# Kernel tuning notes

Hardware: AMD Instinct MI355X
Metric: run time of the kernel (lower is better)

## Reference

```python
import jax, jax.numpy as jnp
import numpy as np
import math

HIDDEN = 1024
HEADS = 16
HEAD_DIM = HIDDEN // HEADS


def setup_inputs() -> dict:
    key = jax.random.key(0)
    k1, k2, k3, k4, k5 = jax.random.split(key, 5)
    B, S = 2, 2048
    scale = 1.0 / math.sqrt(HIDDEN)
    return {
        "batch_hidden": jax.random.normal(k1, (B, S, HIDDEN), dtype=jnp.float32),
        # nn.Linear weights are [out, in]; y = x @ W.T
        "Wq": jax.random.uniform(k2, (HIDDEN, HIDDEN), jnp.float32, -scale, scale),
        "Wk": jax.random.uniform(k3, (HIDDEN, HIDDEN), jnp.float32, -scale, scale),
        "Wg": jax.random.uniform(k4, (HIDDEN, HIDDEN), jnp.float32, -scale, scale),
        "bg": jax.random.uniform(k5, (HIDDEN,), jnp.float32, -scale, scale),
    }


def _split_heads(x):
    # [B,S,H] -> [B,heads,S,head_dim]
    B, S, _ = x.shape
    return x.reshape(B, S, HEADS, HEAD_DIM).transpose(0, 2, 1, 3)


def reference(batch_hidden, Wq, Wk, Wg, bg):
    # NOTE: faithful to source — value uses the KEY projection weights.
    q = batch_hidden @ Wq.T
    k = batch_hidden @ Wk.T
    v = batch_hidden @ Wk.T
    gate = jax.nn.sigmoid(batch_hidden @ Wg.T + bg)  # [B,S,H]

    q = _split_heads(q)  # [B,h,S,d]
    k = _split_heads(k)
    v = _split_heads(v)

    # source: scores = K @ Q^T (softmax over query positions)
    scores = jnp.einsum("bhkd,bhqd->bhkq", k, q) / math.sqrt(HEAD_DIM)
    attn = jax.nn.softmax(scores, axis=-1)  # [B,h,S,S]

    ctx = jnp.einsum("bhkq,bhqd->bhkd", attn, v)  # [B,h,S,d]
    ctx = ctx.transpose(0, 2, 1, 3).reshape(batch_hidden.shape)  # [B,S,H]

    out = gate * ctx
    return out, attn
```

## Files before the change

kernel.cpp:

```cpp
#include <hip/hip_runtime.h>
#include <hip/hip_bf16.h>

#define HID 1024
#define NHEADS 16
#define HDIM 64
#define SEQ 2048
#define NTOK 4096

typedef __attribute__((ext_vector_type(8))) short short8;
typedef __attribute__((ext_vector_type(4))) float f32x4;
typedef unsigned short ush;

__device__ __forceinline__ ush f2bf(float f) {
    unsigned int u = __float_as_uint(f);
    u = (u + 0x7fffu + ((u >> 16) & 1u)) >> 16;
    return (ush)u;
}
__device__ __forceinline__ void async_copy16(const void* g, void* l) {
    __builtin_amdgcn_global_load_lds(
        (const __attribute__((address_space(1))) void*)g,
        (__attribute__((address_space(3))) void*)l, 16, 0, 0);
}
#define SBAR()  __builtin_amdgcn_s_barrier()
#define SCHED() __builtin_amdgcn_sched_barrier(0)

__global__ __launch_bounds__(256) void cvt_kernel(
    const float* __restrict__ X, const float* __restrict__ Wq,
    const float* __restrict__ Wk, const float* __restrict__ Wg,
    ush* __restrict__ Xbf, ush* __restrict__ Wbf)
{
    long i = (long)blockIdx.x * 256 + threadIdx.x;
    const float* src; ush* dst; long j;
    if (i < 524288)      { src = X;  dst = Xbf;           j = i; }
    else if (i < 655360) { src = Wq; dst = Wbf;           j = i - 524288; }
    else if (i < 786432) { src = Wk; dst = Wbf + 1048576; j = i - 655360; }
    else                 { src = Wg; dst = Wbf + 2097152; j = i - 786432; }
    float4 a = *reinterpret_cast<const float4*>(src + j * 8);
    float4 b = *reinterpret_cast<const float4*>(src + j * 8 + 4);
    short8 o;
    o[0] = (short)f2bf(a.x); o[1] = (short)f2bf(a.y);
    o[2] = (short)f2bf(a.z); o[3] = (short)f2bf(a.w);
    o[4] = (short)f2bf(b.x); o[5] = (short)f2bf(b.y);
    o[6] = (short)f2bf(b.z); o[7] = (short)f2bf(b.w);
    *reinterpret_cast<short8*>(dst + j * 8) = o;
}

__global__ __launch_bounds__(256, 3) void proj_kernel(
    const ush* __restrict__ Xbf, const ush* __restrict__ Wbf,
    const float* __restrict__ bgp,
    ush* __restrict__ Qbf, ush* __restrict__ Kbf,
    ush* __restrict__ VtG,
    float* __restrict__ gate)
{
    __shared__ __align__(16) ush As[128 * 64];
    __shared__ __align__(16) ush Bs[128 * 64];

    const int lin = blockIdx.y * 24 + blockIdx.x;
    const int swz = (lin & 7) * 96 + (lin >> 3);
    const int n0 = (swz % 24) * 128;
    const int m0 = (swz / 24) * 128;
    const int tid = threadIdx.x, lane = tid & 63, wv = tid >> 6;
    const int wm = wv >> 1, wn = wv & 1;
    const int l16 = lane & 15, lq = lane >> 4;
    const int lrow = lane >> 3, lc = lane & 7;
    const int scU = lc ^ lrow;
    const int u0 = lq ^ (l16 & 7);

    f32x4 acc[4][4];
    #pragma unroll
    for (int i = 0; i < 4; i++)
        #pragma unroll
        for (int j = 0; j < 4; j++)
            #pragma unroll
            for (int r = 0; r < 4; r++) acc[i][j][r] = 0.0f;

    const ush* gA = Xbf + (long)m0 * HID;
    const ush* gB = Wbf + (long)n0 * HID;

    for (int k0 = 0; k0 < HID; k0 += 64) {
        #pragma unroll
        for (int c = 0; c < 4; ++c) {
            int chunk = wv * 4 + c;
            int row = chunk * 8 + lrow;
            async_copy16(gA + (long)row * HID + k0 + scU * 8, &As[chunk * 512]);
            async_copy16(gB + (long)row * HID + k0 + scU * 8, &Bs[chunk * 512]);
        }
        asm volatile("s_waitcnt vmcnt(0)" ::: "memory");
        SCHED();
        SBAR(); SCHED();
        #pragma unroll
        for (int ks = 0; ks < 2; ++ks) {
            const int uo = (ks ? (u0 ^ 4) : u0) * 8;
            short8 a[4], b[4];
            #pragma unroll
            for (int mf = 0; mf < 4; mf++)
                a[mf] = *reinterpret_cast<const short8*>(&As[(wm * 64 + mf * 16 + l16) * 64 + uo]);
            #pragma unroll
            for (int nf = 0; nf < 4; nf++)
                b[nf] = *reinterpret_cast<const short8*>(&Bs[(wn * 64 + nf * 16 + l16) * 64 + uo]);
            #pragma unroll
            for (int mf = 0; mf < 4; mf++)
                #pragma unroll
                for (int nf = 0; nf < 4; nf++)
                    acc[mf][nf] = __builtin_amdgcn_mfma_f32_16x16x32_bf16(a[mf], b[nf], acc[mf][nf], 0, 0, 0);
        }
        SBAR(); SCHED();
    }

    const int z = n0 >> 10;
    #pragma unroll
    for (int mf = 0; mf < 4; mf++)
        #pragma unroll
        for (int nf = 0; nf < 4; nf++) {
            int row = m0 + wm * 64 + mf * 16 + lq * 4;
            int gcol = n0 + wn * 64 + nf * 16 + l16;
            int col = gcol & 1023;
            #pragma unroll
            for (int r = 0; r < 4; r++) {
                float v = acc[mf][nf][r];
                long idx = (long)(row + r) * HID + col;
                if (z == 0)      Qbf[idx] = f2bf(v * 0.18033688011112042f);
                else if (z == 1) Kbf[idx] = f2bf(v);
                else {
                    float gv = 1.0f / (1.0f + __expf(-(v + bgp[col])));
                    __builtin_nontemporal_store(gv, &gate[idx]);
                }
            }
            if (z == 1) {
                int bb = row >> 11, s = row & 2047;
                int bh = bb * NHEADS + (col >> 6);
                int d  = col & 63;
                unsigned int w0, w1;
                asm volatile("v_cvt_pk_bf16_f32 %0, %1, %2" : "=v"(w0)
                             : "v"(acc[mf][nf][0]), "v"(acc[mf][nf][1]));
                asm volatile("v_cvt_pk_bf16_f32 %0, %1, %2" : "=v"(w1)
                             : "v"(acc[mf][nf][2]), "v"(acc[mf][nf][3]));
                *reinterpret_cast<uint2*>(&VtG[((long)bh * HDIM + d) * SEQ + s]) =
                    make_uint2(w0, w1);
            }
        }
}

__global__ __launch_bounds__(256, 3) void attn_kernel(
    const ush* __restrict__ Qbf,
    const ush* __restrict__ Kbf,
    const ush* __restrict__ VtG,
    float* __restrict__ outp,
    float* __restrict__ attnp)
{
    __shared__ __align__(16) ush QsA[3 * 4096];
    __shared__ __align__(16) ush AtA[128 * 72];
    __shared__ __align__(16) ush VtA[64 * 64];

    ush (*At)[72] = reinterpret_cast<ush(*)[72]>(&AtA[0]);

    const int lin = (blockIdx.z * 16 + blockIdx.y) * 16 + blockIdx.x;
    const int swzb = (lin & 7) * 64 + (lin >> 3);
    const int kblk = swzb & 15;
    const int h    = (swzb >> 4) & 15;
    const int b    = swzb >> 8;
    const int bh   = b * NHEADS + h;
    const int tb   = b * SEQ;
    const int colbase = h * HDIM;
    const int tid  = threadIdx.x;
    const int lane = tid & 63;
    const int wv   = tid >> 6;
    const int l16  = lane & 15, lq = lane >> 4;
    const int lrow = lane >> 3, lc = lane & 7;
    const int scU  = lc ^ lrow;
    const int u0   = lq ^ (l16 & 7);

    const ush* Krow = Kbf + (long)(tb + kblk * 128) * HID + colbase;

    auto stageQ = [&](int q0, int bu) {
        #pragma unroll
        for (int c = 0; c < 2; ++c) {
            int chunk = wv * 2 + c;
            int row = chunk * 8 + lrow;
            async_copy16(Qbf + (long)(tb + q0 + row) * HID + colbase + scU * 8,
                         &QsA[bu * 4096 + chunk * 512]);
        }
    };
    auto stageV = [&](int q0) {
        #pragma unroll
        for (int c = 0; c < 2; ++c) {
            int chunk = wv * 2 + c;
            int row = chunk * 8 + lrow;
            async_copy16(VtG + ((long)bh * HDIM + row) * SEQ + q0 + scU * 8,
                         &VtA[chunk * 512]);
        }
    };

    short8 bk[2][2];
    {
        #pragma unroll
        for (int c = 0; c < 4; ++c) {
            int chunk = wv * 4 + c;
            int row = chunk * 8 + lrow;
            async_copy16(Krow + (long)row * HID + scU * 8, &AtA[chunk * 512]);
        }
        asm volatile("s_waitcnt vmcnt(0)" ::: "memory");
        SCHED();
        SBAR(); SCHED();
        #pragma unroll
        for (int ks = 0; ks < 2; ++ks) {
            const int uo = (ks ? (u0 ^ 4) : u0) * 8;
            #pragma unroll
            for (int nf = 0; nf < 2; ++nf)
                bk[ks][nf] = *reinterpret_cast<const short8*>(
                    &AtA[(wv * 32 + nf * 16 + l16) * 64 + uo]);
        }
        SBAR(); SCHED();
    }

    stageQ(0, 0);
    stageQ(64, 1);

    float ps[2] = {0.0f, 0.0f};

    for (int i = 0; i < 32; ++i) {
        if (i >= 30) asm volatile("s_waitcnt vmcnt(0)" ::: "memory");
        else         asm volatile("s_waitcnt vmcnt(2)" ::: "memory");
        SCHED();
        SBAR(); SCHED();
        if (i < 30) stageQ((i + 2) * 64, (i + 2) % 3);

        f32x4 acc[4][2];
        #pragma unroll
        for (int x = 0; x < 4; x++)
            #pragma unroll
            for (int y = 0; y < 2; y++)
                #pragma unroll
                for (int r = 0; r < 4; r++) acc[x][y][r] = 0.0f;

        const ush* Qb = &QsA[(i % 3) * 4096];
        __builtin_amdgcn_s_setprio(1);
        #pragma unroll
        for (int ks = 0; ks < 2; ks++) {
            const int uo = (ks ? (u0 ^ 4) : u0) * 8;
            short8 aq[4];
            #pragma unroll
            for (int mf = 0; mf < 4; mf++)
                aq[mf] = *reinterpret_cast<const short8*>(&Qb[(mf * 16 + l16) * 64 + uo]);
            #pragma unroll
            for (int mf = 0; mf < 4; mf++)
                #pragma unroll
                for (int nf = 0; nf < 2; nf++)
                    acc[mf][nf] = __builtin_amdgcn_mfma_f32_16x16x32_bf16(aq[mf], bk[ks][nf], acc[mf][nf], 0, 0, 0);
        }
        __builtin_amdgcn_s_setprio(0);

        #pragma unroll
        for (int nf = 0; nf < 2; nf++) {
            float s = 0.0f;
            #pragma unroll
            for (int mf = 0; mf < 4; mf++)
                #pragma unroll
                for (int r = 0; r < 4; r++)
                    s += exp2f(acc[mf][nf][r]);
            ps[nf] += s;
        }
    }

    float inv_r[2];
    #pragma unroll
    for (int nf = 0; nf < 2; nf++) {
        float v = ps[nf];
        v += __shfl_xor(v, 16);
        v += __shfl_xor(v, 32);
        inv_r[nf] = 1.0f / v;
    }

    f32x4 octx[2][4];
    #pragma unroll
    for (int x = 0; x < 2; x++)
        #pragma unroll
        for (int y = 0; y < 4; y++)
            #pragma unroll
            for (int r = 0; r < 4; r++) octx[x][y][r] = 0.0f;

    SBAR();
    stageQ(0, 0);
    stageV(0);
    stageQ(64, 1);

    for (int i = 0; i < 32; ++i) {
        const int q0 = i << 6;
        if (i == 0) asm volatile("s_waitcnt vmcnt(2)" ::: "memory");
        else        asm volatile("s_waitcnt vmcnt(8)" ::: "memory");
        SCHED();
        SBAR(); SCHED();
        if (i < 30) stageQ((i + 2) * 64, (i + 2) % 3);

        f32x4 acc[4][2];
        #pragma unroll
        for (int x = 0; x < 4; x++)
            #pragma unroll
            for (int y = 0; y < 2; y++)
                #pragma unroll
                for (int r = 0; r < 4; r++) acc[x][y][r] = 0.0f;

        const ush* Qb = &QsA[(i % 3) * 4096];
        __builtin_amdgcn_s_setprio(1);
        #pragma unroll
        for (int ks = 0; ks < 2; ks++) {
            const int uo = (ks ? (u0 ^ 4) : u0) * 8;
            short8 aq[4];
            #pragma unroll
            for (int mf = 0; mf < 4; mf++)
                aq[mf] = *reinterpret_cast<const short8*>(&Qb[(mf * 16 + l16) * 64 + uo]);
            #pragma unroll
            for (int mf = 0; mf < 4; mf++)
                #pragma unroll
                for (int nf = 0; nf < 2; nf++)
                    acc[mf][nf] = __builtin_amdgcn_mfma_f32_16x16x32_bf16(aq[mf], bk[ks][nf], acc[mf][nf], 0, 0, 0);
        }
        __builtin_amdgcn_s_setprio(0);

        #pragma unroll
        for (int nf = 0; nf < 2; nf++) {
            const int krl = wv * 32 + nf * 16 + l16;
            const float inv = inv_r[nf];
            #pragma unroll
            for (int mf = 0; mf < 4; mf++) {
                const int qc = mf * 16 + lq * 4;
                float p0 = exp2f(acc[mf][nf][0]) * inv;
                float p1 = exp2f(acc[mf][nf][1]) * inv;
                float p2 = exp2f(acc[mf][nf][2]) * inv;
                float p3 = exp2f(acc[mf][nf][3]) * inv;
                unsigned int w0, w1;
                asm volatile("v_cvt_pk_bf16_f32 %0, %1, %2" : "=v"(w0) : "v"(p0), "v"(p1));
                asm volatile("v_cvt_pk_bf16_f32 %0, %1, %2" : "=v"(w1) : "v"(p2), "v"(p3));
                *reinterpret_cast<uint2*>(&At[krl][qc]) = make_uint2(w0, w1);
            }
        }

        asm volatile("s_waitcnt lgkmcnt(0)" ::: "memory");
        SCHED();

        uint2 wreg[8];
        const int rlo = lane >> 4;
        const int qc  = (lane & 15) * 4;
        #pragma unroll
        for (int j = 0; j < 8; ++j)
            wreg[j] = *reinterpret_cast<const uint2*>(&At[wv * 32 + j * 4 + rlo][qc]);

        __builtin_amdgcn_s_setprio(1);
        #pragma unroll
        for (int ks = 0; ks < 2; ks++) {
            const int uo = (ks ? (u0 ^ 4) : u0) * 8;
            short8 a[2], bv[4];
            #pragma unroll
            for (int mf = 0; mf < 2; mf++)
                a[mf] = *reinterpret_cast<const short8*>(&At[wv * 32 + mf * 16 + l16][ks * 32 + lq * 8]);
            #pragma unroll
            for (int nf = 0; nf < 4; nf++)
                bv[nf] = *reinterpret_cast<const short8*>(&VtA[(nf * 16 + l16) * 64 + uo]);
            #pragma unroll
            for (int mf = 0; mf < 2; mf++)
                #pragma unroll
                for (int nf = 0; nf < 4; nf++)
                    octx[mf][nf] = __builtin_amdgcn_mfma_f32_16x16x32_bf16(a[mf], bv[nf], octx[mf][nf], 0, 0, 0);
        }
        __builtin_amdgcn_s_setprio(0);

        SBAR(); SCHED();
        if (i < 31) stageV((i + 1) * 64);

        #pragma unroll
        for (int j = 0; j < 8; ++j) {
            const int rl = wv * 32 + j * 4 + rlo;
            f32x4 st;
            st[0] = __uint_as_float(wreg[j].x << 16);
            st[1] = __uint_as_float(wreg[j].x & 0xffff0000u);
            st[2] = __uint_as_float(wreg[j].y << 16);
            st[3] = __uint_as_float(wreg[j].y & 0xffff0000u);
            __builtin_nontemporal_store(st,
                reinterpret_cast<f32x4*>(attnp + ((long)bh * SEQ + kblk * 128 + rl) * SEQ + q0 + qc));
        }
    }

    #pragma unroll
    for (int mf = 0; mf < 2; mf++)
        #pragma unroll
        for (int nf = 0; nf < 4; nf++) {
            int row = tb + kblk * 128 + wv * 32 + mf * 16 + lq * 4;
            int col = colbase + nf * 16 + l16;
            #pragma unroll
            for (int r = 0; r < 4; r++) {
                long idx = (long)(row + r) * HID + col;
                float g = __builtin_nontemporal_load(&outp[idx]);
                __builtin_nontemporal_store(g * octx[mf][nf][r], &outp[idx]);
            }
        }
}

extern "C" void kernel_launch(void* const* d_in, const int* in_sizes, int n_in,
                              void* d_out, int out_size, void* d_ws, size_t ws_size,
                              hipStream_t stream)
{
    const float* X  = (const float*)d_in[0];
    const float* Wq = (const float*)d_in[1];
    const float* Wk = (const float*)d_in[2];
    const float* Wg = (const float*)d_in[3];
    const float* bg = (const float*)d_in[4];

    float* outp  = (float*)d_out;
    float* attnp = outp + (long)NTOK * HID;

    ush* Qbf = (ush*)d_ws;
    ush* Kbf = Qbf + (long)NTOK * HID;
    ush* VtG = Kbf + (long)NTOK * HID;

    ush* Xbf = (ush*)(outp + 134742016L);
    ush* Wbf = Xbf + (long)NTOK * HID;

    cvt_kernel<<<3584, 256, 0, stream>>>(X, Wq, Wk, Wg, Xbf, Wbf);
    proj_kernel<<<dim3(24, 32), 256, 0, stream>>>(Xbf, Wbf, bg, Qbf, Kbf, VtG, outp);
    attn_kernel<<<dim3(16, 16, 2), 256, 0, stream>>>(Qbf, Kbf, VtG, outp, attnp);
}
```

Baseline: 214.2 us.

## Split attention block into two 64-row halves and overlap second half's row-sum pass

Each block still handles 128 key rows, now as two 64-row halves (a and b) processed in sequence instead of one 128-row pass. The row-sum pass for half b is folded into half a's output pass, which drops one full QK^T sweep. The change also shrinks the At buffer and lowers the launch bound from 3 to 2 blocks per CU. In exchange it duplicates code, recomputes QK for half b in both passes, and runs fewer waves per CU.

```diff
diff --git a/kernel.cpp b/kernel.cpp
--- a/kernel.cpp
+++ b/kernel.cpp
@@ -141,7 +141,7 @@
         }
 }
 
-__global__ __launch_bounds__(256, 3) void attn_kernel(
+__global__ __launch_bounds__(256, 2) void attn_kernel(
     const ush* __restrict__ Qbf,
     const ush* __restrict__ Kbf,
     const ush* __restrict__ VtG,
@@ -149,89 +149,81 @@
     float* __restrict__ attnp)
 {
     __shared__ __align__(16) ush QsA[3 * 4096];
-    __shared__ __align__(16) ush AtA[128 * 72];
+    __shared__ __align__(16) ush AtA[64 * 72];
     __shared__ __align__(16) ush VtA[64 * 64];
 
     ush (*At)[72] = reinterpret_cast<ush(*)[72]>(&AtA[0]);
 
-    const int lin = (blockIdx.z * 16 + blockIdx.y) * 16 + blockIdx.x;
+    const int lin  = blockIdx.x;
     const int swzb = (lin & 7) * 64 + (lin >> 3);
-    const int kblk = swzb & 15;
+    const int rh   = swzb & 1;
+    const int pair = (swzb >> 1) & 7;
     const int h    = (swzb >> 4) & 15;
     const int b    = swzb >> 8;
     const int bh   = b * NHEADS + h;
     const int tb   = b * SEQ;
     const int colbase = h * HDIM;
+    const int rowbase_a = pair * 256 + rh * 64;
+    const int rowbase_b = rowbase_a + 128;
+
     const int tid  = threadIdx.x;
     const int lane = tid & 63;
     const int wv   = tid >> 6;
     const int l16  = lane & 15, lq = lane >> 4;
-    const int lrow = lane >> 3, lc = lane & 7;
-    const int scU  = lc ^ lrow;
     const int u0   = lq ^ (l16 & 7);
-
-    const ush* Krow = Kbf + (long)(tb + kblk * 128) * HID + colbase;
-
-    auto stageQ = [&](int q0, int bu) {
+    const int rlo  = lane >> 4;
+    const int qc2  = (lane & 15) * 4;
+
+    auto stageT = [&](const ush* src, long stride, ush* dst) {
         #pragma unroll
         for (int c = 0; c < 2; ++c) {
-            int chunk = wv * 2 + c;
-            int row = chunk * 8 + lrow;
-            async_copy16(Qbf + (long)(tb + q0 + row) * HID + colbase + scU * 8,
-                         &QsA[bu * 4096 + chunk * 512]);
+            int p = c * 256 + tid;
+            int row = p >> 3, lc2 = p & 7;
+            int scU2 = lc2 ^ (row & 7);
+            async_copy16(src + (long)row * stride + scU2 * 8, dst + c * 2048 + wv * 512);
         }
     };
-    auto stageV = [&](int q0) {
-        #pragma unroll
-        for (int c = 0; c < 2; ++c) {
-            int chunk = wv * 2 + c;
-            int row = chunk * 8 + lrow;
-            async_copy16(VtG + ((long)bh * HDIM + row) * SEQ + q0 + scU * 8,
-                         &VtA[chunk * 512]);
-        }
-    };
-
-    short8 bk[2][2];
+    const ush* Qsrc = Qbf + (long)tb * HID + colbase;
+    const ush* Vsrc = VtG + (long)bh * HDIM * SEQ;
+
+    short8 bk_a[2], bk_b[2];
     {
-        #pragma unroll
-        for (int c = 0; c < 4; ++c) {
-            int chunk = wv * 4 + c;
-            int row = chunk * 8 + lrow;
-            async_copy16(Krow + (long)row * HID + scU * 8, &AtA[chunk * 512]);
-        }
-        asm volatile("s_waitcnt vmcnt(0)" ::: "memory");
-        SCHED();
+        stageT(Kbf + (long)(tb + rowbase_a) * HID + colbase, HID, AtA);
+        asm volatile("s_waitcnt vmcnt(0)" ::: "memory"); SCHED();
         SBAR(); SCHED();
         #pragma unroll
         for (int ks = 0; ks < 2; ++ks) {
             const int uo = (ks ? (u0 ^ 4) : u0) * 8;
-            #pragma unroll
-            for (int nf = 0; nf < 2; ++nf)
-                bk[ks][nf] = *reinterpret_cast<const short8*>(
-                    &AtA[(wv * 32 + nf * 16 + l16) * 64 + uo]);
-        }
-        SBAR(); SCHED();
-    }
-
-    stageQ(0, 0);
-    stageQ(64, 1);
-
-    float ps[2] = {0.0f, 0.0f};
-
+            bk_a[ks] = *reinterpret_cast<const short8*>(&AtA[(wv * 16 + l16) * 64 + uo]);
+        }
+        SBAR(); SCHED();
+        stageT(Kbf + (long)(tb + rowbase_b) * HID + colbase, HID, AtA);
+        asm volatile("s_waitcnt vmcnt(0)" ::: "memory"); SCHED();
+        SBAR(); SCHED();
+        #pragma unroll
+        for (int ks = 0; ks < 2; ++ks) {
+            const int uo = (ks ? (u0 ^ 4) : u0) * 8;
+            bk_b[ks] = *reinterpret_cast<const short8*>(&AtA[(wv * 16 + l16) * 64 + uo]);
+        }
+        SBAR(); SCHED();
+    }
+
+    stageT(Qsrc, HID, &QsA[0]);
+    stageT(Qsrc + (long)64 * HID, HID, &QsA[4096]);
+
+    float ps_a = 0.0f;
     for (int i = 0; i < 32; ++i) {
         if (i >= 30) asm volatile("s_waitcnt vmcnt(0)" ::: "memory");
         else         asm volatile("s_waitcnt vmcnt(2)" ::: "memory");
         SCHED();
         SBAR(); SCHED();
-        if (i < 30) stageQ((i + 2) * 64, (i + 2) % 3);
-
-        f32x4 acc[4][2];
+        if (i < 30) stageT(Qsrc + (long)((i + 2) * 64) * HID, HID, &QsA[((i + 2) % 3) * 4096]);
+
+        f32x4 acc[4];
         #pragma unroll
         for (int x = 0; x < 4; x++)
             #pragma unroll
-            for (int y = 0; y < 2; y++)
-                #pragma unroll
-                for (int r = 0; r < 4; r++) acc[x][y][r] = 0.0f;
+            for (int r = 0; r < 4; r++) acc[x][r] = 0.0f;
 
         const ush* Qb = &QsA[(i % 3) * 4096];
         __builtin_amdgcn_s_setprio(1);
@@ -244,61 +236,51 @@
                 aq[mf] = *reinterpret_cast<const short8*>(&Qb[(mf * 16 + l16) * 64 + uo]);
             #pragma unroll
             for (int mf = 0; mf < 4; mf++)
-                #pragma unroll
-                for (int nf = 0; nf < 2; nf++)
-                    acc[mf][nf] = __builtin_amdgcn_mfma_f32_16x16x32_bf16(aq[mf], bk[ks][nf], acc[mf][nf], 0, 0, 0);
+                acc[mf] = __builtin_amdgcn_mfma_f32_16x16x32_bf16(aq[mf], bk_a[ks], acc[mf], 0, 0, 0);
         }
         __builtin_amdgcn_s_setprio(0);
 
         #pragma unroll
-        for (int nf = 0; nf < 2; nf++) {
+        for (int mf = 0; mf < 4; mf++) {
             float s = 0.0f;
             #pragma unroll
-            for (int mf = 0; mf < 4; mf++)
-                #pragma unroll
-                for (int r = 0; r < 4; r++)
-                    s += exp2f(acc[mf][nf][r]);
-            ps[nf] += s;
-        }
-    }
-
-    float inv_r[2];
-    #pragma unroll
-    for (int nf = 0; nf < 2; nf++) {
-        float v = ps[nf];
+            for (int r = 0; r < 4; r++) s += exp2f(acc[mf][r]);
+            ps_a += s;
+        }
+    }
+    float inv_a;
+    {
+        float v = ps_a;
         v += __shfl_xor(v, 16);
         v += __shfl_xor(v, 32);
-        inv_r[nf] = 1.0f / v;
-    }
-
-    f32x4 octx[2][4];
+        inv_a = 1.0f / v;
+    }
+
+    SBAR();
+    stageT(Qsrc, HID, &QsA[0]);
+    stageT(Vsrc, SEQ, VtA);
+    stageT(Qsrc + (long)64 * HID, HID, &QsA[4096]);
+
+    float ps_b = 0.0f;
+    f32x4 octx[4];
     #pragma unroll
-    for (int x = 0; x < 2; x++)
-        #pragma unroll
-        for (int y = 0; y < 4; y++)
-            #pragma unroll
-            for (int r = 0; r < 4; r++) octx[x][y][r] = 0.0f;
-
-    SBAR();
-    stageQ(0, 0);
-    stageV(0);
-    stageQ(64, 1);
+    for (int y = 0; y < 4; y++)
+        #pragma unroll
+        for (int r = 0; r < 4; r++) octx[y][r] = 0.0f;
 
     for (int i = 0; i < 32; ++i) {
         const int q0 = i << 6;
-        if (i == 0) asm volatile("s_waitcnt vmcnt(2)" ::: "memory");
-        else        asm volatile("s_waitcnt vmcnt(8)" ::: "memory");
+        if (i == 0) asm volatile("s_waitcnt vmcnt(0)" ::: "memory");
+        else        asm volatile("s_waitcnt vmcnt(4)" ::: "memory");
         SCHED();
         SBAR(); SCHED();
-        if (i < 30) stageQ((i + 2) * 64, (i + 2) % 3);
-
-        f32x4 acc[4][2];
+        if (i < 30) stageT(Qsrc + (long)((i + 2) * 64) * HID, HID, &QsA[((i + 2) % 3) * 4096]);
+
+        f32x4 aA[4], aB[4];
         #pragma unroll
         for (int x = 0; x < 4; x++)
             #pragma unroll
-            for (int y = 0; y < 2; y++)
-                #pragma unroll
-                for (int r = 0; r < 4; r++) acc[x][y][r] = 0.0f;
+            for (int r = 0; r < 4; r++) { aA[x][r] = 0.0f; aB[x][r] = 0.0f; }
 
         const ush* Qb = &QsA[(i % 3) * 4096];
         __builtin_amdgcn_s_setprio(1);
@@ -311,88 +293,191 @@
                 aq[mf] = *reinterpret_cast<const short8*>(&Qb[(mf * 16 + l16) * 64 + uo]);
             #pragma unroll
             for (int mf = 0; mf < 4; mf++)
-                #pragma unroll
-                for (int nf = 0; nf < 2; nf++)
-                    acc[mf][nf] = __builtin_amdgcn_mfma_f32_16x16x32_bf16(aq[mf], bk[ks][nf], acc[mf][nf], 0, 0, 0);
+                aA[mf] = __builtin_amdgcn_mfma_f32_16x16x32_bf16(aq[mf], bk_a[ks], aA[mf], 0, 0, 0);
+            #pragma unroll
+            for (int mf = 0; mf < 4; mf++)
+                aB[mf] = __builtin_amdgcn_mfma_f32_16x16x32_bf16(aq[mf], bk_b[ks], aB[mf], 0, 0, 0);
         }
         __builtin_amdgcn_s_setprio(0);
 
-        #pragma unroll
-        for (int nf = 0; nf < 2; nf++) {
-            const int krl = wv * 32 + nf * 16 + l16;
-            const float inv = inv_r[nf];
+        {
+            const int krl = wv * 16 + l16;
             #pragma unroll
             for (int mf = 0; mf < 4; mf++) {
                 const int qc = mf * 16 + lq * 4;
-                float p0 = exp2f(acc[mf][nf][0]) * inv;
-                float p1 = exp2f(acc[mf][nf][1]) * inv;
-                float p2 = exp2f(acc[mf][nf][2]) * inv;
-                float p3 = exp2f(acc[mf][nf][3]) * inv;
+                float p0 = exp2f(aA[mf][0]) * inv_a;
+                float p1 = exp2f(aA[mf][1]) * inv_a;
+                float p2 = exp2f(aA[mf][2]) * inv_a;
+                float p3 = exp2f(aA[mf][3]) * inv_a;
                 unsigned int w0, w1;
                 asm volatile("v_cvt_pk_bf16_f32 %0, %1, %2" : "=v"(w0) : "v"(p0), "v"(p1));
                 asm volatile("v_cvt_pk_bf16_f32 %0, %1, %2" : "=v"(w1) : "v"(p2), "v"(p3));
                 *reinterpret_cast<uint2*>(&At[krl][qc]) = make_uint2(w0, w1);
             }
         }
-
         asm volatile("s_waitcnt lgkmcnt(0)" ::: "memory");
         SCHED();
 
-        uint2 wreg[8];
-        const int rlo = lane >> 4;
-        const int qc  = (lane & 15) * 4;
-        #pragma unroll
-        for (int j = 0; j < 8; ++j)
-            wreg[j] = *reinterpret_cast<const uint2*>(&At[wv * 32 + j * 4 + rlo][qc]);
+        uint2 wreg[4];
+        #pragma unroll
+        for (int j = 0; j < 4; ++j)
+            wreg[j] = *reinterpret_cast<const uint2*>(&At[wv * 16 + j * 4 + rlo][qc2]);
 
         __builtin_amdgcn_s_setprio(1);
         #pragma unroll
         for (int ks = 0; ks < 2; ks++) {
             const int uo = (ks ? (u0 ^ 4) : u0) * 8;
-            short8 a[2], bv[4];
-            #pragma unroll
-            for (int mf = 0; mf < 2; mf++)
-                a[mf] = *reinterpret_cast<const short8*>(&At[wv * 32 + mf * 16 + l16][ks * 32 + lq * 8]);
-            #pragma unroll
-            for (int nf = 0; nf < 4; nf++)
-                bv[nf] = *reinterpret_cast<const short8*>(&VtA[(nf * 16 + l16) * 64 + uo]);
-            #pragma unroll
-            for (int mf = 0; mf < 2; mf++)
-                #pragma unroll
-                for (int nf = 0; nf < 4; nf++)
-                    octx[mf][nf] = __builtin_amdgcn_mfma_f32_16x16x32_bf16(a[mf], bv[nf], octx[mf][nf], 0, 0, 0);
+            short8 a = *reinterpret_cast<const short8*>(&At[wv * 16 + l16][ks * 32 + lq * 8]);
+            #pragma unroll
+            for (int nf = 0; nf < 4; nf++) {
+                short8 bv = *reinterpret_cast<const short8*>(&VtA[(nf * 16 + l16) * 64 + uo]);
+                octx[nf] = __builtin_amdgcn_mfma_f32_16x16x32_bf16(a, bv, octx[nf], 0, 0, 0);
+            }
         }
         __builtin_amdgcn_s_setprio(0);
 
-        SBAR(); SCHED();
-        if (i < 31) stageV((i + 1) * 64);
-
-        #pragma unroll
-        for (int j = 0; j < 8; ++j) {
-            const int rl = wv * 32 + j * 4 + rlo;
+        #pragma unroll
+        for (int mf = 0; mf < 4; mf++) {
+            float s = 0.0f;
+            #pragma unroll
+            for (int r = 0; r < 4; r++) s += exp2f(aB[mf][r]);
+            ps_b += s;
+        }
+
+        SBAR(); SCHED();
+        if (i < 31) stageT(Vsrc + (i + 1) * 64, SEQ, VtA);
+
+        #pragma unroll
+        for (int j = 0; j < 4; ++j) {
+            const int rl = rowbase_a + wv * 16 + j * 4 + rlo;
             f32x4 st;
             st[0] = __uint_as_float(wreg[j].x << 16);
             st[1] = __uint_as_float(wreg[j].x & 0xffff0000u);
             st[2] = __uint_as_float(wreg[j].y << 16);
             st[3] = __uint_as_float(wreg[j].y & 0xffff0000u);
             __builtin_nontemporal_store(st,
-                reinterpret_cast<f32x4*>(attnp + ((long)bh * SEQ + kblk * 128 + rl) * SEQ + q0 + qc));
-        }
+                reinterpret_cast<f32x4*>(attnp + ((long)bh * SEQ + rl) * SEQ + q0 + qc2));
+        }
+    }
+    float inv_b;
+    {
+        float v = ps_b;
+        v += __shfl_xor(v, 16);
+        v += __shfl_xor(v, 32);
+        inv_b = 1.0f / v;
     }
 
     #pragma unroll
-    for (int mf = 0; mf < 2; mf++)
-        #pragma unroll
-        for (int nf = 0; nf < 4; nf++) {
-            int row = tb + kblk * 128 + wv * 32 + mf * 16 + lq * 4;
-            int col = colbase + nf * 16 + l16;
-            #pragma unroll
-            for (int r = 0; r < 4; r++) {
-                long idx = (long)(row + r) * HID + col;
-                float g = __builtin_nontemporal_load(&outp[idx]);
-                __builtin_nontemporal_store(g * octx[mf][nf][r], &outp[idx]);
+    for (int nf = 0; nf < 4; nf++) {
+        int col = colbase + nf * 16 + l16;
+        #pragma unroll
+        for (int r = 0; r < 4; r++) {
+            long idx = (long)(tb + rowbase_a + wv * 16 + lq * 4 + r) * HID + col;
+            float g = __builtin_nontemporal_load(&outp[idx]);
+            __builtin_nontemporal_store(g * octx[nf][r], &outp[idx]);
+        }
+    }
+
+    stageT(Qsrc, HID, &QsA[0]);
+    stageT(Vsrc, SEQ, VtA);
+    stageT(Qsrc + (long)64 * HID, HID, &QsA[4096]);
+
+    #pragma unroll
+    for (int y = 0; y < 4; y++)
+        #pragma unroll
+        for (int r = 0; r < 4; r++) octx[y][r] = 0.0f;
+
+    for (int i = 0; i < 32; ++i) {
+        const int q0 = i << 6;
+        if (i == 0) asm volatile("s_waitcnt vmcnt(0)" ::: "memory");
+        else        asm volatile("s_waitcnt vmcnt(4)" ::: "memory");
+        SCHED();
+        SBAR(); SCHED();
+        if (i < 30) stageT(Qsrc + (long)((i + 2) * 64) * HID, HID, &QsA[((i + 2) % 3) * 4096]);
+
+        f32x4 aB[4];
+        #pragma unroll
+        for (int x = 0; x < 4; x++)
+            #pragma unroll
+            for (int r = 0; r < 4; r++) aB[x][r] = 0.0f;
+
+        const ush* Qb = &QsA[(i % 3) * 4096];
+        __builtin_amdgcn_s_setprio(1);
+        #pragma unroll
+        for (int ks = 0; ks < 2; ks++) {
+            const int uo = (ks ? (u0 ^ 4) : u0) * 8;
+            short8 aq[4];
+            #pragma unroll
+            for (int mf = 0; mf < 4; mf++)
+                aq[mf] = *reinterpret_cast<const short8*>(&Qb[(mf * 16 + l16) * 64 + uo]);
+            #pragma unroll
+            for (int mf = 0; mf < 4; mf++)
+                aB[mf] = __builtin_amdgcn_mfma_f32_16x16x32_bf16(aq[mf], bk_b[ks], aB[mf], 0, 0, 0);
+        }
+        __builtin_amdgcn_s_setprio(0);
+
+        {
+            const int krl = wv * 16 + l16;
+            #pragma unroll
+            for (int mf = 0; mf < 4; mf++) {
+                const int qc = mf * 16 + lq * 4;
+                float p0 = exp2f(aB[mf][0]) * inv_b;
+                float p1 = exp2f(aB[mf][1]) * inv_b;
+                float p2 = exp2f(aB[mf][2]) * inv_b;
+                float p3 = exp2f(aB[mf][3]) * inv_b;
+                unsigned int w0, w1;
+                asm volatile("v_cvt_pk_bf16_f32 %0, %1, %2" : "=v"(w0) : "v"(p0), "v"(p1));
+                asm volatile("v_cvt_pk_bf16_f32 %0, %1, %2" : "=v"(w1) : "v"(p2), "v"(p3));
+                *reinterpret_cast<uint2*>(&At[krl][qc]) = make_uint2(w0, w1);
             }
         }
+        asm volatile("s_waitcnt lgkmcnt(0)" ::: "memory");
+        SCHED();
+
+        uint2 wreg[4];
+        #pragma unroll
+        for (int j = 0; j < 4; ++j)
+            wreg[j] = *reinterpret_cast<const uint2*>(&At[wv * 16 + j * 4 + rlo][qc2]);
+
+        __builtin_amdgcn_s_setprio(1);
+        #pragma unroll
+        for (int ks = 0; ks < 2; ks++) {
+            const int uo = (ks ? (u0 ^ 4) : u0) * 8;
+            short8 a = *reinterpret_cast<const short8*>(&At[wv * 16 + l16][ks * 32 + lq * 8]);
+            #pragma unroll
+            for (int nf = 0; nf < 4; nf++) {
+                short8 bv = *reinterpret_cast<const short8*>(&VtA[(nf * 16 + l16) * 64 + uo]);
+                octx[nf] = __builtin_amdgcn_mfma_f32_16x16x32_bf16(a, bv, octx[nf], 0, 0, 0);
+            }
+        }
+        __builtin_amdgcn_s_setprio(0);
+
+        SBAR(); SCHED();
+        if (i < 31) stageT(Vsrc + (i + 1) * 64, SEQ, VtA);
+
+        #pragma unroll
+        for (int j = 0; j < 4; ++j) {
+            const int rl = rowbase_b + wv * 16 + j * 4 + rlo;
+            f32x4 st;
+            st[0] = __uint_as_float(wreg[j].x << 16);
+            st[1] = __uint_as_float(wreg[j].x & 0xffff0000u);
+            st[2] = __uint_as_float(wreg[j].y << 16);
+            st[3] = __uint_as_float(wreg[j].y & 0xffff0000u);
+            __builtin_nontemporal_store(st,
+                reinterpret_cast<f32x4*>(attnp + ((long)bh * SEQ + rl) * SEQ + q0 + qc2));
+        }
+    }
+
+    #pragma unroll
+    for (int nf = 0; nf < 4; nf++) {
+        int col = colbase + nf * 16 + l16;
+        #pragma unroll
+        for (int r = 0; r < 4; r++) {
+            long idx = (long)(tb + rowbase_b + wv * 16 + lq * 4 + r) * HID + col;
+            float g = __builtin_nontemporal_load(&outp[idx]);
+            __builtin_nontemporal_store(g * octx[nf][r], &outp[idx]);
+        }
+    }
 }
 
 extern "C" void kernel_launch(void* const* d_in, const int* in_sizes, int n_in,
@@ -417,5 +502,5 @@
 
     cvt_kernel<<<3584, 256, 0, stream>>>(X, Wq, Wk, Wg, Xbf, Wbf);
     proj_kernel<<<dim3(24, 32), 256, 0, stream>>>(Xbf, Wbf, bg, Qbf, Kbf, VtG, outp);
-    attn_kernel<<<dim3(16, 16, 2), 256, 0, stream>>>(Qbf, Kbf, VtG, outp, attnp);
+    attn_kernel<<<512, 256, 0, stream>>>(Qbf, Kbf, VtG, outp, attnp);
 }
```

Result: faster. 206.2 us (-3.8%).
